# Optimization experiments

Hardware: AMD Instinct MI355X
Metric: run time of the kernel (lower is better)

Reference implementation:

```python
import jax, jax.numpy as jnp
import numpy as np


def setup_inputs() -> dict:
    key = jax.random.key(0)
    k_x, k_enc, k_dec = jax.random.split(key, 3)
    B, T, d_in, d_sae = 2048, 4, 768, 16384
    x = jax.random.normal(k_x, (B, T, d_in), dtype=jnp.float32)
    W_enc = jax.random.normal(k_enc, (T, d_in, d_sae), dtype=jnp.float32) * (1.0 / d_in ** 0.5)
    W_dec = jax.random.normal(k_dec, (d_sae, T, d_in), dtype=jnp.float32) * (1.0 / d_sae ** 0.5)
    b_enc = jnp.zeros((d_sae,), dtype=jnp.float32)
    b_dec = jnp.zeros((T, d_in), dtype=jnp.float32)
    return {"x": x, "W_enc": W_enc, "b_enc": b_enc, "W_dec": W_dec, "b_dec": b_dec, "k": 128}


def reference(x, W_enc, b_enc, W_dec, b_dec, k):
    # pre-activations: (B, d_sae)
    pre = jnp.einsum('btd,tds->bs', x, W_enc) + b_enc
    # top-k selection along dictionary dim, then relu + scatter into zero vector
    vals, idx = jax.lax.top_k(pre, k)                      # (B, k)
    B = pre.shape[0]
    rows = jnp.arange(B)[:, None]                          # (B, 1)
    z = jnp.zeros_like(pre).at[rows, idx].set(jax.nn.relu(vals))  # (B, d_sae)
    # dense decode (original ignores sparsity of z)
    x_hat = jnp.einsum('bs,std->btd', z, W_dec) + b_dec    # (B, T, d_in)
    recon_loss = jnp.mean(jnp.sum((x_hat - x) ** 2, axis=-1))
    return (recon_loss, x_hat, z)
```

## Files before the change

### kernel.cpp

```cpp
#include <hip/hip_runtime.h>
#include <hip/hip_bf16.h>

#define B_ROWS 2048
#define K_DIM  3072
#define N_DIM  16384
#define TOPK   128
#define XHAT_ELEMS (B_ROWS * K_DIM)

typedef __bf16 bf16x8 __attribute__((ext_vector_type(8)));
typedef float  f32x4  __attribute__((ext_vector_type(4)));

#define LDSTRIDE 40

__device__ __forceinline__ unsigned bf16rne(float f) {
    unsigned u = __float_as_uint(f);
    unsigned r = u + 0x7fffu + ((u >> 16) & 1u);
    return r & 0xffff0000u;
}
__device__ __forceinline__ unsigned pk2_rne(float x, float y) {
    return (bf16rne(x) >> 16) | bf16rne(y);
}
__device__ __forceinline__ float lo16f(unsigned u) { return __uint_as_float(u << 16); }
__device__ __forceinline__ float hi16f(unsigned u) { return __uint_as_float(u & 0xffff0000u); }

__global__ __launch_bounds__(256) void enc_gemm_mfma(const float* __restrict__ X,
                                                     const float* __restrict__ W,
                                                     const float* __restrict__ benc,
                                                     float* __restrict__ pre) {
    __shared__ unsigned short Ahi[128 * LDSTRIDE], Alo[128 * LDSTRIDE];
    __shared__ unsigned short Bhi[128 * LDSTRIDE], Blo[128 * LDSTRIDE];

    const int t   = threadIdx.x;
    const int bid = blockIdx.x;
    const int mt  = bid & 15;
    const int nt  = bid >> 4;
    const int m0  = mt * 128, n0 = nt * 128;

    int am[4], akq[4], bn[4], bkq[4];
    const float* Xp[4];
    const float* Wp[4];
#pragma unroll
    for (int i = 0; i < 4; ++i) {
        int id = t + 256 * i;
        am[i]  = id >> 3;
        akq[i] = id & 7;
        Xp[i]  = X + (size_t)(m0 + am[i]) * K_DIM + akq[i] * 4;
        bn[i]  = id & 127;
        bkq[i] = id >> 7;
        Wp[i]  = W + (size_t)(bkq[i] * 4) * N_DIM + n0 + bn[i];
    }

    f32x4 acc[4][4];
#pragma unroll
    for (int mi = 0; mi < 4; ++mi)
#pragma unroll
        for (int ni = 0; ni < 4; ++ni) acc[mi][ni] = (f32x4)0.f;

    float4 aR[4];
    float  bR[4][4];
#pragma unroll
    for (int i = 0; i < 4; ++i) {
        aR[i] = *(const float4*)(Xp[i]);
#pragma unroll
        for (int j = 0; j < 4; ++j) bR[i][j] = Wp[i][(size_t)j * N_DIM];
    }

    const int w = t >> 6, lane = t & 63;
    const int wm = (w >> 1) * 64, wn = (w & 1) * 64;
    const int fm = lane & 15, fk = lane >> 4;

    for (int k0 = 0; k0 < K_DIM; k0 += 32) {
        __syncthreads();
#pragma unroll
        for (int i = 0; i < 4; ++i) {
            float4 v = aR[i];
            unsigned h0 = pk2_rne(v.x, v.y), h1 = pk2_rne(v.z, v.w);
            unsigned l0 = pk2_rne(v.x - lo16f(h0), v.y - hi16f(h0));
            unsigned l1 = pk2_rne(v.z - lo16f(h1), v.w - hi16f(h1));
            int off = am[i] * LDSTRIDE + akq[i] * 4;
            uint2 uh; uh.x = h0; uh.y = h1;
            uint2 ul; ul.x = l0; ul.y = l1;
            *(uint2*)&Ahi[off] = uh;
            *(uint2*)&Alo[off] = ul;

            float w0 = bR[i][0], w1 = bR[i][1], w2 = bR[i][2], w3 = bR[i][3];
            unsigned g0 = pk2_rne(w0, w1), g1 = pk2_rne(w2, w3);
            unsigned m0u = pk2_rne(w0 - lo16f(g0), w1 - hi16f(g0));
            unsigned m1u = pk2_rne(w2 - lo16f(g1), w3 - hi16f(g1));
            int boff = bn[i] * LDSTRIDE + bkq[i] * 4;
            uint2 gh; gh.x = g0; gh.y = g1;
            uint2 gl; gl.x = m0u; gl.y = m1u;
            *(uint2*)&Bhi[boff] = gh;
            *(uint2*)&Blo[boff] = gl;
        }
        __syncthreads();

        if (k0 + 32 < K_DIM) {
#pragma unroll
            for (int i = 0; i < 4; ++i) {
                aR[i] = *(const float4*)(Xp[i] + (k0 + 32));
                const float* p = Wp[i] + (size_t)(k0 + 32) * N_DIM;
#pragma unroll
                for (int j = 0; j < 4; ++j) bR[i][j] = p[(size_t)j * N_DIM];
            }
        }

        bf16x8 aH[4], aL[4];
#pragma unroll
        for (int mi = 0; mi < 4; ++mi) {
            int r = (wm + mi * 16 + fm) * LDSTRIDE + fk * 8;
            aH[mi] = *(const bf16x8*)&Ahi[r];
            aL[mi] = *(const bf16x8*)&Alo[r];
        }
#pragma unroll
        for (int ni = 0; ni < 4; ++ni) {
            int r = (wn + ni * 16 + fm) * LDSTRIDE + fk * 8;
            bf16x8 bH = *(const bf16x8*)&Bhi[r];
            bf16x8 bL = *(const bf16x8*)&Blo[r];
#pragma unroll
            for (int mi = 0; mi < 4; ++mi) {
                acc[mi][ni] = __builtin_amdgcn_mfma_f32_16x16x32_bf16(aH[mi], bH, acc[mi][ni], 0, 0, 0);
                acc[mi][ni] = __builtin_amdgcn_mfma_f32_16x16x32_bf16(aH[mi], bL, acc[mi][ni], 0, 0, 0);
                acc[mi][ni] = __builtin_amdgcn_mfma_f32_16x16x32_bf16(aL[mi], bH, acc[mi][ni], 0, 0, 0);
            }
        }
    }

    const int frow = fk * 4, fcol = fm;
#pragma unroll
    for (int ni = 0; ni < 4; ++ni) {
        int col = n0 + wn + ni * 16 + fcol;
        float bv = benc[col];
#pragma unroll
        for (int mi = 0; mi < 4; ++mi) {
            int row = m0 + wm + mi * 16 + frow;
            float* p = pre + (size_t)row * N_DIM + col;
#pragma unroll
            for (int r = 0; r < 4; ++r) p[(size_t)r * N_DIM] = acc[mi][ni][r] + bv;
        }
    }
}

__device__ __forceinline__ unsigned sortkey(float f) {
    unsigned u = __float_as_uint(f);
    return (u & 0x80000000u) ? ~u : (u | 0x80000000u);
}

__device__ __forceinline__ int wave_red_int(int v) {
#pragma unroll
    for (int o = 32; o > 0; o >>= 1) v += __shfl_xor(v, o);
    return v;
}

__global__ __launch_bounds__(256) void topk_kernel(float* __restrict__ z,
                                                   int* __restrict__ oIdx,
                                                   float* __restrict__ oVal) {
    __shared__ unsigned short k16[N_DIM];
    __shared__ int s4[4];
    __shared__ int s_candN;
    __shared__ int s_candIdx[256];
    __shared__ unsigned s_candKey[256];
    __shared__ int s_quota;
    __shared__ int s_outPos;

    const int row = blockIdx.x;
    const int t = threadIdx.x;
    float* zr = z + (size_t)row * N_DIM;

    if (t == 0) { s_candN = 0; s_outPos = 0; }

    for (int i = t; i < N_DIM; i += 256) {
        k16[i] = (unsigned short)(sortkey(zr[i]) >> 16);
    }
    __syncthreads();

    unsigned cur = 0;
    for (int bit = 15; bit >= 0; --bit) {
        unsigned cand = cur | (1u << bit);
        int c = 0;
        for (int i = t; i < N_DIM; i += 256) c += (k16[i] >= cand) ? 1 : 0;
        c = wave_red_int(c);
        __syncthreads();
        if ((t & 63) == 0) s4[t >> 6] = c;
        __syncthreads();
        int total = s4[0] + s4[1] + s4[2] + s4[3];
        if (total >= TOPK) cur = cand;
    }

    {
        int c = 0;
        for (int i = t; i < N_DIM; i += 256) c += (k16[i] > cur) ? 1 : 0;
        c = wave_red_int(c);
        __syncthreads();
        if ((t & 63) == 0) s4[t >> 6] = c;
        __syncthreads();
        int cgt = s4[0] + s4[1] + s4[2] + s4[3];
        if (t == 0) s_quota = TOPK - cgt;
    }
    __syncthreads();

    for (int i = t; i < N_DIM; i += 256) {
        if (k16[i] == (unsigned short)cur) {
            int p = atomicAdd(&s_candN, 1);
            if (p < 256) {
                s_candIdx[p] = i;
                s_candKey[p] = sortkey(zr[i]);
            }
        }
    }
    __syncthreads();

    if (t == 0) {
        int n = s_candN < 256 ? s_candN : 256;
        int q = s_quota;
        if (q > n) q = n;
        s_quota = q;
        for (int a = 0; a < q; ++a) {
            int best = a;
            for (int b = a + 1; b < n; ++b) {
                if (s_candKey[b] > s_candKey[best] ||
                    (s_candKey[b] == s_candKey[best] && s_candIdx[b] < s_candIdx[best]))
                    best = b;
            }
            if (best != a) {
                unsigned tk = s_candKey[a]; s_candKey[a] = s_candKey[best]; s_candKey[best] = tk;
                int ti = s_candIdx[a]; s_candIdx[a] = s_candIdx[best]; s_candIdx[best] = ti;
            }
        }
    }
    __syncthreads();

    const int quota = s_quota;
    for (int i = t; i < N_DIM; i += 256) {
        float f = zr[i];
        unsigned short kk = k16[i];
        bool sel = kk > (unsigned short)cur;
        if (!sel && kk == (unsigned short)cur) {
            for (int j = 0; j < quota; ++j)
                if (s_candIdx[j] == i) { sel = true; break; }
        }
        float zv = sel ? fmaxf(f, 0.f) : 0.f;
        zr[i] = zv;
        if (sel) {
            int p = atomicAdd(&s_outPos, 1);
            oIdx[row * TOPK + p] = i;
            oVal[row * TOPK + p] = zv;
        }
    }
}

__global__ __launch_bounds__(256) void decode_kernel(const int* __restrict__ idxL,
                                                     const float* __restrict__ valL,
                                                     const float* __restrict__ Wdec,
                                                     const float* __restrict__ bdec,
                                                     const float* __restrict__ x,
                                                     float* __restrict__ xhat,
                                                     float* __restrict__ loss) {
    __shared__ int s_idx[TOPK];
    __shared__ float s_val[TOPK];
    __shared__ float sred[4];

    const int row = blockIdx.x;
    const int t = threadIdx.x;

    if (t < TOPK) {
        s_idx[t] = idxL[row * TOPK + t];
        s_val[t] = valL[row * TOPK + t];
    }
    __syncthreads();

    float acc[12];
#pragma unroll
    for (int e = 0; e < 12; ++e) acc[e] = bdec[t + e * 256];

    for (int i = 0; i < TOPK; ++i) {
        const float v = s_val[i];
        const float* wr = Wdec + (size_t)s_idx[i] * K_DIM;
#pragma unroll
        for (int e = 0; e < 12; ++e)
            acc[e] = fmaf(v, wr[t + e * 256], acc[e]);
    }

    const float* xr = x + (size_t)row * K_DIM;
    float* xo = xhat + (size_t)row * K_DIM;
    float part = 0.f;
#pragma unroll
    for (int e = 0; e < 12; ++e) {
        float d = acc[e] - xr[t + e * 256];
        part = fmaf(d, d, part);
        xo[t + e * 256] = acc[e];
    }

#pragma unroll
    for (int o = 32; o > 0; o >>= 1) part += __shfl_xor(part, o);
    if ((t & 63) == 0) sred[t >> 6] = part;
    __syncthreads();
    if (t == 0) {
        float total = sred[0] + sred[1] + sred[2] + sred[3];
        atomicAdd(loss, total * (1.0f / 8192.0f));
    }
}

extern "C" void kernel_launch(void* const* d_in, const int* in_sizes, int n_in,
                              void* d_out, int out_size, void* d_ws, size_t ws_size,
                              hipStream_t stream) {
    const float* x     = (const float*)d_in[0];
    const float* W_enc = (const float*)d_in[1];
    const float* b_enc = (const float*)d_in[2];
    const float* W_dec = (const float*)d_in[3];
    const float* b_dec = (const float*)d_in[4];

    float* out  = (float*)d_out;
    float* loss = out;
    float* xhat = out + 1;
    float* z    = out + 1 + XHAT_ELEMS;

    int*   oIdx = (int*)d_ws;
    float* oVal = (float*)((char*)d_ws + (size_t)B_ROWS * TOPK * sizeof(int));

    (void)hipMemsetAsync(loss, 0, sizeof(float), stream);

    enc_gemm_mfma<<<2048, 256, 0, stream>>>(x, W_enc, b_enc, z);

    topk_kernel<<<B_ROWS, 256, 0, stream>>>(z, oIdx, oVal);

    decode_kernel<<<B_ROWS, 256, 0, stream>>>(oIdx, oVal, W_dec, b_dec, x, xhat, loss);
}
```

Measured before the change: 1.726 ms.

## Pre-split encoder operands into bf16 hi/lo planes and load via global_load_lds

Adds two prepass kernels. One splits x into bf16 hi/lo planes, and the other transposes W_enc into K-major bf16 hi/lo planes. A new encoder GEMM then streams these planes into swizzled LDS with direct global-to-LDS loads and runs three bf16 MFMAs per tile step. This removes the per-tile fp32-to-bf16 split and transposition from the GEMM inner loop and halves the bytes the GEMM loads per operand plane. In exchange it adds extra passes that read and write about 200MB of W planes per call, and it only runs when the workspace is large enough.

```diff
diff --git a/kernel.cpp b/kernel.cpp
--- a/kernel.cpp
+++ b/kernel.cpp
@@ -22,6 +22,158 @@
 }
 __device__ __forceinline__ float lo16f(unsigned u) { return __uint_as_float(u << 16); }
 __device__ __forceinline__ float hi16f(unsigned u) { return __uint_as_float(u & 0xffff0000u); }
+
+__device__ __forceinline__ int swz4(int r) { return (r ^ (r >> 2)) & 3; }
+
+__device__ __forceinline__ void gl_lds16(const void* g, void* l) {
+    __builtin_amdgcn_global_load_lds((__attribute__((address_space(1))) const void*)g,
+                                     (__attribute__((address_space(3))) void*)l, 16, 0, 0);
+}
+
+__global__ __launch_bounds__(256) void split_x_kernel(const float* __restrict__ X,
+                                                      unsigned short* __restrict__ Xh,
+                                                      unsigned short* __restrict__ Xl) {
+    size_t i = ((size_t)blockIdx.x * 256 + threadIdx.x) * 8;
+    float4 a = *(const float4*)(X + i);
+    float4 b = *(const float4*)(X + i + 4);
+    unsigned h0 = pk2_rne(a.x, a.y), h1 = pk2_rne(a.z, a.w);
+    unsigned h2 = pk2_rne(b.x, b.y), h3 = pk2_rne(b.z, b.w);
+    unsigned l0 = pk2_rne(a.x - lo16f(h0), a.y - hi16f(h0));
+    unsigned l1 = pk2_rne(a.z - lo16f(h1), a.w - hi16f(h1));
+    unsigned l2 = pk2_rne(b.x - lo16f(h2), b.y - hi16f(h2));
+    unsigned l3 = pk2_rne(b.z - lo16f(h3), b.w - hi16f(h3));
+    uint4 hv; hv.x = h0; hv.y = h1; hv.z = h2; hv.w = h3;
+    uint4 lv; lv.x = l0; lv.y = l1; lv.z = l2; lv.w = l3;
+    *(uint4*)(Xh + i) = hv;
+    *(uint4*)(Xl + i) = lv;
+}
+
+__global__ __launch_bounds__(256) void split_wT_kernel(const float* __restrict__ W,
+                                                       unsigned short* __restrict__ WhT,
+                                                       unsigned short* __restrict__ WlT) {
+    __shared__ float s[64][65];
+    const int t  = threadIdx.x;
+    const int k0 = blockIdx.x * 64;
+    const int n0 = blockIdx.y * 64;
+    const int c4 = t & 15, r = t >> 4;
+
+#pragma unroll
+    for (int p = 0; p < 4; ++p) {
+        int rr = r + p * 16;
+        float4 v = *(const float4*)(W + (size_t)(k0 + rr) * N_DIM + n0 + c4 * 4);
+        s[rr][c4 * 4 + 0] = v.x;
+        s[rr][c4 * 4 + 1] = v.y;
+        s[rr][c4 * 4 + 2] = v.z;
+        s[rr][c4 * 4 + 3] = v.w;
+    }
+    __syncthreads();
+#pragma unroll
+    for (int p = 0; p < 4; ++p) {
+        int rr = r + p * 16;
+        float v0 = s[c4 * 4 + 0][rr];
+        float v1 = s[c4 * 4 + 1][rr];
+        float v2 = s[c4 * 4 + 2][rr];
+        float v3 = s[c4 * 4 + 3][rr];
+        unsigned h01 = pk2_rne(v0, v1), h23 = pk2_rne(v2, v3);
+        unsigned l01 = pk2_rne(v0 - lo16f(h01), v1 - hi16f(h01));
+        unsigned l23 = pk2_rne(v2 - lo16f(h23), v3 - hi16f(h23));
+        size_t o = (size_t)(n0 + rr) * K_DIM + k0 + c4 * 4;
+        uint2 hv; hv.x = h01; hv.y = h23;
+        uint2 lv; lv.x = l01; lv.y = l23;
+        *(uint2*)(WhT + o) = hv;
+        *(uint2*)(WlT + o) = lv;
+    }
+}
+
+__global__ __launch_bounds__(256) void enc_gemm_presplit(
+        const unsigned short* __restrict__ Xh, const unsigned short* __restrict__ Xl,
+        const unsigned short* __restrict__ WhT, const unsigned short* __restrict__ WlT,
+        const float* __restrict__ benc, float* __restrict__ pre) {
+    __shared__ unsigned short Ah[128 * 32], Al[128 * 32];
+    __shared__ unsigned short Bh[128 * 32], Bl[128 * 32];
+
+    const int t   = threadIdx.x;
+    const int bid = blockIdx.x;
+    const int mt  = bid & 15;
+    const int nt  = bid >> 4;
+    const int m0  = mt * 128, n0 = nt * 128;
+
+    const int sr = t >> 2;
+    const int sc = ((t & 3) ^ swz4(sr)) * 8;
+    const size_t rstep = (size_t)64 * K_DIM;
+
+    const unsigned short* xh0 = Xh  + (size_t)(m0 + sr) * K_DIM + sc;
+    const unsigned short* xl0 = Xl  + (size_t)(m0 + sr) * K_DIM + sc;
+    const unsigned short* wh0 = WhT + (size_t)(n0 + sr) * K_DIM + sc;
+    const unsigned short* wl0 = WlT + (size_t)(n0 + sr) * K_DIM + sc;
+
+    unsigned short* ahD0 = &Ah[(size_t)t * 8];
+    unsigned short* ahD1 = &Ah[(size_t)(t + 256) * 8];
+    unsigned short* alD0 = &Al[(size_t)t * 8];
+    unsigned short* alD1 = &Al[(size_t)(t + 256) * 8];
+    unsigned short* bhD0 = &Bh[(size_t)t * 8];
+    unsigned short* bhD1 = &Bh[(size_t)(t + 256) * 8];
+    unsigned short* blD0 = &Bl[(size_t)t * 8];
+    unsigned short* blD1 = &Bl[(size_t)(t + 256) * 8];
+
+    f32x4 acc[4][4];
+#pragma unroll
+    for (int mi = 0; mi < 4; ++mi)
+#pragma unroll
+        for (int ni = 0; ni < 4; ++ni) acc[mi][ni] = (f32x4)0.f;
+
+    const int w = t >> 6, lane = t & 63;
+    const int wm = (w >> 1) * 64, wn = (w & 1) * 64;
+    const int fm = lane & 15, fk = lane >> 4;
+    const int koff = (fk ^ swz4(fm)) * 8;
+
+    for (int k0 = 0; k0 < K_DIM; k0 += 32) {
+        __syncthreads();
+        gl_lds16(xh0 + k0,         ahD0);
+        gl_lds16(xh0 + k0 + rstep, ahD1);
+        gl_lds16(xl0 + k0,         alD0);
+        gl_lds16(xl0 + k0 + rstep, alD1);
+        gl_lds16(wh0 + k0,         bhD0);
+        gl_lds16(wh0 + k0 + rstep, bhD1);
+        gl_lds16(wl0 + k0,         blD0);
+        gl_lds16(wl0 + k0 + rstep, blD1);
+        __syncthreads();
+
+        bf16x8 aH[4], aL[4];
+#pragma unroll
+        for (int mi = 0; mi < 4; ++mi) {
+            int r = (wm + mi * 16 + fm) * 32 + koff;
+            aH[mi] = *(const bf16x8*)&Ah[r];
+            aL[mi] = *(const bf16x8*)&Al[r];
+        }
+#pragma unroll
+        for (int ni = 0; ni < 4; ++ni) {
+            int r = (wn + ni * 16 + fm) * 32 + koff;
+            bf16x8 bH = *(const bf16x8*)&Bh[r];
+            bf16x8 bL = *(const bf16x8*)&Bl[r];
+#pragma unroll
+            for (int mi = 0; mi < 4; ++mi) {
+                acc[mi][ni] = __builtin_amdgcn_mfma_f32_16x16x32_bf16(aH[mi], bH, acc[mi][ni], 0, 0, 0);
+                acc[mi][ni] = __builtin_amdgcn_mfma_f32_16x16x32_bf16(aH[mi], bL, acc[mi][ni], 0, 0, 0);
+                acc[mi][ni] = __builtin_amdgcn_mfma_f32_16x16x32_bf16(aL[mi], bH, acc[mi][ni], 0, 0, 0);
+            }
+        }
+    }
+
+    const int frow = fk * 4, fcol = fm;
+#pragma unroll
+    for (int ni = 0; ni < 4; ++ni) {
+        int col = n0 + wn + ni * 16 + fcol;
+        float bv = benc[col];
+#pragma unroll
+        for (int mi = 0; mi < 4; ++mi) {
+            int row = m0 + wm + mi * 16 + frow;
+            float* p = pre + (size_t)row * N_DIM + col;
+#pragma unroll
+            for (int r = 0; r < 4; ++r) p[(size_t)r * N_DIM] = acc[mi][ni][r] + bv;
+        }
+    }
+}
 
 __global__ __launch_bounds__(256) void enc_gemm_mfma(const float* __restrict__ X,
                                                      const float* __restrict__ W,
@@ -315,12 +467,28 @@
     float* xhat = out + 1;
     float* z    = out + 1 + XHAT_ELEMS;
 
+    const size_t idxB   = (size_t)B_ROWS * TOPK * sizeof(int);
+    const size_t planeW = (size_t)K_DIM * N_DIM * 2;
+    const size_t planeX = (size_t)B_ROWS * K_DIM * 2;
+    const size_t need   = 2 * idxB + 2 * planeW + 2 * planeX;
+
     int*   oIdx = (int*)d_ws;
-    float* oVal = (float*)((char*)d_ws + (size_t)B_ROWS * TOPK * sizeof(int));
+    float* oVal = (float*)((char*)d_ws + idxB);
 
     (void)hipMemsetAsync(loss, 0, sizeof(float), stream);
 
-    enc_gemm_mfma<<<2048, 256, 0, stream>>>(x, W_enc, b_enc, z);
+    if (ws_size >= need) {
+        unsigned short* WhT = (unsigned short*)((char*)d_ws + 2 * idxB);
+        unsigned short* WlT = (unsigned short*)((char*)WhT + planeW);
+        unsigned short* Xh  = (unsigned short*)((char*)WlT + planeW);
+        unsigned short* Xl  = (unsigned short*)((char*)Xh + planeX);
+
+        split_x_kernel<<<(B_ROWS * K_DIM) / (8 * 256), 256, 0, stream>>>(x, Xh, Xl);
+        split_wT_kernel<<<dim3(K_DIM / 64, N_DIM / 64), 256, 0, stream>>>(W_enc, WhT, WlT);
+        enc_gemm_presplit<<<2048, 256, 0, stream>>>(Xh, Xl, WhT, WlT, b_enc, z);
+    } else {
+        enc_gemm_mfma<<<2048, 256, 0, stream>>>(x, W_enc, b_enc, z);
+    }
 
     topk_kernel<<<B_ROWS, 256, 0, stream>>>(z, oIdx, oVal);
 
```

Measured after the change: 1.607 ms. 1.07x faster.
